# Performance work log

Hardware: AMD Instinct MI355X
Metric: run time of the kernel (lower is better)

## Reference

```python
import jax, jax.numpy as jnp
import numpy as np

N_QUBITS = 10
DIM = 2 ** N_QUBITS          # quantum state dimension
N_LAYERS = 8                 # QAOA circuit depth
B, D_IN, D_HID = 8192, 1024, 2048


def _build_hamiltonians(key):
    """Faithful to _create_cost_hamiltonian / _create_mixer_hamiltonian."""
    k1, k2 = jax.random.split(key)
    # cost: random diagonal * 0.1 plus 100 nearest-neighbour real couplings * 0.05
    diag = (jax.random.normal(k1, (DIM,)) * 0.1).astype(jnp.complex64)
    Hc = jnp.zeros((DIM, DIM), jnp.complex64).at[jnp.arange(DIM), jnp.arange(DIM)].set(diag)
    i = jnp.arange(100)
    j = (i + 1) % DIM
    c = (jax.random.normal(k2, (100,)) * 0.05).astype(jnp.complex64)
    Hc = Hc.at[i, j].set(c).at[j, i].set(jnp.conj(c))
    # mixer: sum of Pauli-X on every qubit -> H[i, i^(1<<q)] += 1
    idx = jnp.arange(DIM)
    Hm = jnp.zeros((DIM, DIM), jnp.complex64)
    for q in range(N_QUBITS):
        Hm = Hm.at[idx, idx ^ (1 << q)].add(1.0)
    return Hc, Hm


def setup_inputs() -> dict:
    key = jax.random.key(0)
    ks = jax.random.split(key, 8)
    Hc, Hm = _build_hamiltonians(ks[0])
    s = lambda k, *sh: jax.random.normal(k, sh, jnp.float32)
    return {
        "x": s(ks[1], B, D_IN),
        "W1": s(ks[2], D_IN, D_HID) * 0.02, "b1": jnp.zeros((D_HID,), jnp.float32),
        "W2": s(ks[3], D_HID, D_HID // 2) * 0.02, "b2": jnp.zeros((D_HID // 2,), jnp.float32),
        "Wq": s(ks[4], N_QUBITS, D_HID // 2) * 0.02, "bq": jnp.zeros((D_HID // 2,), jnp.float32),
        "Wo": s(ks[5], D_HID // 2, D_IN) * 0.02, "bo": jnp.zeros((D_IN,), jnp.float32),
        "circuit_params": s(ks[6], 2 * N_LAYERS),
        "Hc": Hc, "Hm": Hm,
    }


def _qaoa_params(circuit_params, Hc, Hm):
    """QuantumApproximateOptimizer.optimize_parameters: layered unitary evolution
    then a projective measurement mapped to +/-1 parameters."""
    state = jnp.full((DIM,), 1.0 / np.sqrt(DIM), jnp.complex64)
    for l in range(N_LAYERS):  # small fixed layer count -> Python loop OK
        gamma = circuit_params[2 * l].astype(jnp.complex64)
        beta = circuit_params[2 * l + 1].astype(jnp.complex64)
        state = jax.scipy.linalg.expm(-1j * gamma * Hc) @ state
        state = jax.scipy.linalg.expm(-1j * beta * Hm) @ state
    probs = jnp.abs(state) ** 2
    m = jax.random.categorical(jax.random.key(42), jnp.log(probs + 1e-30))
    # format(m, '0{n}b') is MSB-first
    bits = (m >> jnp.arange(N_QUBITS - 1, -1, -1)) & 1
    return bits.astype(jnp.float32) * 2.0 - 1.0  # +/-1 per qubit


def reference(x, W1, b1, W2, b2, Wq, bq, Wo, bo, circuit_params, Hc, Hm):
    # classical encoder: Linear -> ReLU -> Linear
    feat = jax.nn.relu(x @ W1 + b1) @ W2 + b2          # [B, D_HID//2]
    # quantum branch (batch independent)
    qp = _qaoa_params(circuit_params, Hc, Hm)          # [N_QUBITS]
    # surface-code error correction: correction_lookup only maps syndromes
    # '0000'/'1111' to qubit indices 23/24, which fail the `qubit_idx < param_dim`
    # guard for param_dim = N_QUBITS -> provably a no-op; qp unchanged.
    qf = qp @ Wq + bq                                  # [D_HID//2]
    return (feat + qf) @ Wo + bo                       # [B, D_IN]
```

## Files before the change

kernel.cpp:

```cpp
#include <hip/hip_runtime.h>
#include <hip/hip_bf16.h>
#include <stdint.h>

#define DIM 1024
#define NQ 10
#define NLAYERS 8
#define KTAYLOR 16
#define B_ROWS 8192
#define D_IN 1024
#define D_HID 2048
#define D_HALF 1024

typedef __bf16 bf16x8 __attribute__((ext_vector_type(8)));
typedef float f32x4 __attribute__((ext_vector_type(4)));

__device__ __forceinline__ float ldany(const void* p, size_t i, bool f32) {
  if (f32) return ((const float*)p)[i];
  return (float)((const __bf16*)p)[i];
}

__device__ __forceinline__ uint16_t f2bf_bits(float f) {
  __bf16 v = (__bf16)f;
  return *(uint16_t*)&v;
}

__global__ void detect_kernel(const uint32_t* __restrict__ w1raw,
                              const uint32_t* __restrict__ hc,
                              int* __restrict__ flags) {
  if (threadIdx.x == 0) {
    int cnt = 0;
    for (int i = 0; i < 256; ++i) {
      uint16_t h = (uint16_t)(w1raw[i] & 0xFFFFu);
      if (((h >> 7) & 0xFF) >= 0x80) cnt++;
    }
    flags[0] = (cnt > 32) ? 1 : 0;

    uint32_t w1 = hc[1] & 0x7FFFFFFFu;
    uint32_t w2 = hc[2] & 0x7FFFFFFFu;
    uint32_t w1025 = hc[1025] & 0x7FFFFFFFu;
    int code;
    if (w2 != 0u) code = 1;
    else if (w1 != 0u && (w1 >> 16) == 0u) code = 3;
    else if (w1025 != 0u) code = 2;
    else if (w1 != 0u) code = 4;
    else code = 0;
    flags[1] = code;
  }
}

__global__ __launch_bounds__(256) void convert_bf16(
    const void* __restrict__ src, size_t soff, __bf16* __restrict__ dst,
    int n, const int* __restrict__ flags) {
  int i = (blockIdx.x * 256 + threadIdx.x) * 8;
  if (i >= n) return;
  if (flags[0]) {
    const float* s = (const float*)src + soff + i;
#pragma unroll
    for (int j = 0; j < 8; ++j) dst[i + j] = (__bf16)s[j];
  } else {
    *(uint4*)(dst + i) = *(const uint4*)((const uint16_t*)src + soff + i);
  }
}

__device__ __forceinline__ uint32_t rotl32(uint32_t v, int d) {
  return (v << d) | (v >> (32 - d));
}

__device__ inline void threefry2x32(uint32_t k0, uint32_t k1, uint32_t& x0, uint32_t& x1) {
  uint32_t ks2 = k0 ^ k1 ^ 0x1BD11BDAu;
  x0 += k0; x1 += k1;
#define RND(r) { x0 += x1; x1 = rotl32(x1, r); x1 ^= x0; }
  RND(13) RND(15) RND(26) RND(6)
  x0 += k1; x1 += ks2 + 1u;
  RND(17) RND(29) RND(16) RND(24)
  x0 += ks2; x1 += k0 + 2u;
  RND(13) RND(15) RND(26) RND(6)
  x0 += k0; x1 += k1 + 3u;
  RND(17) RND(29) RND(16) RND(24)
  x0 += k1; x1 += ks2 + 4u;
  RND(13) RND(15) RND(26) RND(6)
  x0 += ks2; x1 += k0 + 5u;
#undef RND
}

__device__ __forceinline__ float gumbel_from_bits(uint32_t b) {
  float f = __uint_as_float((b >> 9) | 0x3f800000u) - 1.0f;
  float u = fmaxf(f, 1.17549435e-38f);
  return -__logf(-__logf(u));
}

struct cplx { double r, i; };
__device__ __forceinline__ cplx load_hc(const void* H, int code, size_t idx) {
  switch (code) {
    case 2: return {(double)((const float*)H)[idx], 0.0};
    case 3: {
      const uint16_t* h = (const uint16_t*)H;
      return {(double)__uint_as_float((uint32_t)h[2 * idx] << 16),
              (double)__uint_as_float((uint32_t)h[2 * idx + 1] << 16)};
    }
    case 4: {
      const double* d = (const double*)H;
      return {d[2 * idx], d[2 * idx + 1]};
    }
    default: {
      float2 v = ((const float2*)H)[idx];
      return {(double)v.x, (double)v.y};
    }
  }
}

__global__ __launch_bounds__(1024) void qaoa_kernel(
    const void* __restrict__ Hc_raw, const void* __restrict__ cp,
    const void* __restrict__ b1, const void* __restrict__ b2,
    const void* __restrict__ bq, const void* __restrict__ bo,
    const void* __restrict__ Wq, const int* __restrict__ flags,
    float* __restrict__ b1f, float* __restrict__ bias2, float* __restrict__ bof,
    int* __restrict__ diag) {
  __shared__ double2 Sb[2][DIM];
  __shared__ double gtab[NLAYERS], cbt[NLAYERS], sbt[NLAYERS];
  __shared__ float red_v[16];
  __shared__ int   red_i[16];
  __shared__ float red_p[16];
  __shared__ int bm_sh;

  const int t = threadIdx.x;
  const int lane = t & 63, wave = t >> 6;
  const bool f32 = (flags[0] != 0);
  const int code = flags[1];

  cplx dg = load_hc(Hc_raw, code, (size_t)t * DIM + t);

  cplx tdg0{0,0}, tdg1{0,0}, tcu0{0,0}, tcu1{0,0}, tcd0{0,0}, tcd1{0,0};
  if (wave == 0 && lane <= 50) {
    const size_t e0 = 2 * lane, e1 = 2 * lane + 1;
    tdg0 = load_hc(Hc_raw, code, e0 * DIM + e0);
    tdg1 = load_hc(Hc_raw, code, e1 * DIM + e1);
    if (e0 <= 100) tcu0 = load_hc(Hc_raw, code, e0 * DIM + e0 + 1);
    if (e1 <= 100) tcu1 = load_hc(Hc_raw, code, e1 * DIM + e1 + 1);
    if (e0 >= 1 && e0 <= 100) tcd0 = load_hc(Hc_raw, code, e0 * DIM + e0 - 1);
    if (e1 <= 100) tcd1 = load_hc(Hc_raw, code, e1 * DIM + e1 - 1);
  }

  if (t < NLAYERS) {
    gtab[t] = (double)ldany(cp, 2 * t, f32);
    double b = (double)ldany(cp, 2 * t + 1, f32);
    double s, c;
    sincos(b, &s, &c);
    cbt[t] = c; sbt[t] = s;
  }

  double ar = 0.03125, ai = 0.0;
  __syncthreads();

  for (int l = 0; l < NLAYERS; ++l) {
    const double gamma = gtab[l];
    const double cb = cbt[l], sb_ = sbt[l];

    Sb[0][t] = make_double2(ar, ai);
    __syncthreads();
    if (t >= 102) {
      float af_ = (float)(gamma * dg.r);
      double sn = (double)__sinf(af_), cs = (double)__cosf(af_);
      double sc_ = (dg.i == 0.0) ? 1.0 : exp(gamma * dg.i);
      double nr = sc_ * (ar * cs + ai * sn);
      double ni = sc_ * (ai * cs - ar * sn);
      ar = nr; ai = ni;
    } else if (wave == 0) {
      const double gd0r = gamma * tdg0.r, gd0i = gamma * tdg0.i;
      const double gd1r = gamma * tdg1.r, gd1i = gamma * tdg1.i;
      const double gu0r = gamma * tcu0.r, gu0i = gamma * tcu0.i;
      const double gu1r = gamma * tcu1.r, gu1i = gamma * tcu1.i;
      const double gc0r = gamma * tcd0.r, gc0i = gamma * tcd0.i;
      const double gc1r = gamma * tcd1.r, gc1i = gamma * tcd1.i;
      double p0r = 0, p0i = 0, p1r = 0, p1i = 0;
      if (lane <= 50) {
        double2 v0 = Sb[0][2 * lane], v1 = Sb[0][2 * lane + 1];
        p0r = v0.x; p0i = v0.y; p1r = v1.x; p1i = v1.y;
      }
      double y0r = p0r, y0i = p0i, y1r = p1r, y1i = p1i;
#pragma unroll
      for (int k = 1; k <= KTAYLOR; ++k) {
        double dnr = __shfl_up(p1r, 1), dni = __shfl_up(p1i, 1);
        double upr = __shfl_down(p0r, 1), upi = __shfl_down(p0i, 1);
        double h0r = gd0r * p0r - gd0i * p0i + gu0r * p1r - gu0i * p1i
                   + gc0r * dnr - gc0i * dni;
        double h0i = gd0r * p0i + gd0i * p0r + gu0r * p1i + gu0i * p1r
                   + gc0r * dni + gc0i * dnr;
        double h1r = gd1r * p1r - gd1i * p1i + gu1r * upr - gu1i * upi
                   + gc1r * p0r - gc1i * p0i;
        double h1i = gd1r * p1i + gd1i * p1r + gu1r * upi + gu1i * upr
                   + gc1r * p0i + gc1i * p0r;
        const double s = 1.0 / (double)k;
        p0r = s * h0i; p0i = -s * h0r;
        p1r = s * h1i; p1i = -s * h1r;
        y0r += p0r; y0i += p0i; y1r += p1r; y1i += p1i;
      }
      if (lane <= 50) {
        Sb[0][2 * lane]     = make_double2(y0r, y0i);
        Sb[0][2 * lane + 1] = make_double2(y1r, y1i);
      }
    }
    __syncthreads();
    if (t <= 101) { double2 v = Sb[0][t]; ar = v.x; ai = v.y; }

#pragma unroll
    for (int q = 0; q < 6; ++q) {
      double br_ = __shfl_xor(ar, 1 << q);
      double bi_ = __shfl_xor(ai, 1 << q);
      double nr = cb * ar + sb_ * bi_;
      double ni = cb * ai - sb_ * br_;
      ar = nr; ai = ni;
    }
    int s = 0;
#pragma unroll
    for (int q = 6; q < 10; ++q) {
      Sb[s][t] = make_double2(ar, ai);
      __syncthreads();
      double2 b = Sb[s][t ^ (1 << q)];
      double nr = cb * ar + sb_ * b.y;
      double ni = cb * ai - sb_ * b.x;
      ar = nr; ai = ni;
      s ^= 1;
    }
  }

  double prob = ar * ar + ai * ai;
  float pv = (float)prob;
  float score;
  {
    float logit = __logf((float)prob + 1e-30f);
    uint32_t x0 = 0u, x1 = (uint32_t)t;
    threefry2x32(0u, 42u, x0, x1);
    score = logit + gumbel_from_bits(x0 ^ x1);
  }
  int idx = t;
#pragma unroll
  for (int off = 32; off >= 1; off >>= 1) {
    float ov = __shfl_down(score, off);
    int oi = __shfl_down(idx, off);
    pv += __shfl_down(pv, off);
    if (ov > score) { score = ov; idx = oi; }
  }
  if (lane == 0) { red_v[wave] = score; red_i[wave] = idx; red_p[wave] = pv; }
  __syncthreads();
  if (t == 0) {
    float best = red_v[0]; int bm = red_i[0]; float total = red_p[0];
    for (int w = 1; w < 16; ++w) {
      total += red_p[w];
      if (red_v[w] > best) { best = red_v[w]; bm = red_i[w]; }
    }
    bm_sh = bm;
    diag[0] = (!(total > 0.99f && total < 1.01f)) ? 1 : 0;
    diag[1] = bm;
  }
  __syncthreads();
  const int m = bm_sh;

  float acc = ldany(b2, t, f32) + ldany(bq, t, f32);
#pragma unroll
  for (int k = 0; k < NQ; ++k) {
    float qp = ((m >> (9 - k)) & 1) ? 1.f : -1.f;
    acc += qp * ldany(Wq, k * D_HALF + t, f32);
  }
  bias2[t] = acc;
  bof[t] = ldany(bo, t, f32);
  b1f[t] = ldany(b1, t, f32);
  b1f[t + 1024] = ldany(b1, t + 1024, f32);
}

__global__ void sentinel_kernel(const int* __restrict__ flags,
                                const int* __restrict__ diag,
                                float* __restrict__ out) {
  if (threadIdx.x == 0 && (diag[0] || flags[1] == 0)) {
    out[0] = 1048576.0f + 4194304.0f * (float)diag[0]
           + 65536.0f * (float)flags[1] + 16.0f * (float)diag[1];
  }
}

__global__ __launch_bounds__(256) void transpose_any(
    const void* __restrict__ in, uint16_t* __restrict__ out, int R, int C,
    const int* __restrict__ flags) {
  __shared__ uint16_t tile[32][33];
  const bool f32 = (flags[0] != 0);
  int bc = blockIdx.x * 32, br = blockIdx.y * 32;
  int x = threadIdx.x, y = threadIdx.y;
#pragma unroll
  for (int i = 0; i < 4; ++i) {
    int r = y * 4 + i;
    size_t idx = (size_t)(br + r) * C + bc + x;
    tile[r][x] = f32 ? f2bf_bits(((const float*)in)[idx])
                     : ((const uint16_t*)in)[idx];
  }
  __syncthreads();
#pragma unroll
  for (int i = 0; i < 4; ++i) {
    int c = y * 4 + i;
    out[(size_t)(bc + c) * R + br + x] = tile[x][c];
  }
}

__device__ __forceinline__ void stage_tile(
    const __bf16* __restrict__ G, int row0, int K, int k0,
    __bf16* lds, int wave, int lane) {
#pragma unroll
  for (int r = 0; r < 2; ++r) {
    int e = r * 2048 + wave * 512 + lane * 8;
    int row = e >> 5, col = e & 31;
    const __bf16* gp = G + (size_t)(row0 + row) * K + k0 + col;
    __builtin_amdgcn_global_load_lds(
        (const __attribute__((address_space(1))) void*)gp,
        (__attribute__((address_space(3))) void*)(lds + r * 2048 + wave * 512),
        16, 0, 0);
  }
}

template <bool RELU, bool OUTF32>
__global__ __launch_bounds__(256) void gemm_bt(
    const __bf16* __restrict__ A, const __bf16* __restrict__ Bt,
    const float* __restrict__ bias, void* __restrict__ Cout,
    int N, int K) {
  __shared__ __bf16 Als[2][128 * 32];
  __shared__ __bf16 Bls[2][128 * 32];

  const int tid = threadIdx.x;
  const int wave = tid >> 6, lane = tid & 63;

  const int gx = gridDim.x;
  const int nwg = gx * gridDim.y;
  int flat = blockIdx.y * gx + blockIdx.x;
  const int chunk = nwg >> 3;
  flat = (flat & 7) * chunk + (flat >> 3);
  const int m0 = (flat / gx) * 128, n0 = (flat % gx) * 128;

  const int wm = (wave >> 1) * 64, wn = (wave & 1) * 64;
  const int lm = lane & 15, quad = lane >> 4;

  f32x4 acc[4][4] = {};

  const int nt = K >> 5;
  stage_tile(A,  m0, K, 0, Als[0], wave, lane);
  stage_tile(Bt, n0, K, 0, Bls[0], wave, lane);
  __syncthreads();

  for (int t = 0; t < nt; ++t) {
    const int cur = t & 1;
    if (t + 1 < nt) {
      stage_tile(A,  m0, K, (t + 1) << 5, Als[cur ^ 1], wave, lane);
      stage_tile(Bt, n0, K, (t + 1) << 5, Bls[cur ^ 1], wave, lane);
    }

    bf16x8 af[4], bfr[4];
#pragma unroll
    for (int i = 0; i < 4; ++i)
      af[i] = *(const bf16x8*)(Als[cur] + (wm + i * 16 + lm) * 32 + quad * 8);
#pragma unroll
    for (int i = 0; i < 4; ++i)
      bfr[i] = *(const bf16x8*)(Bls[cur] + (wn + i * 16 + lm) * 32 + quad * 8);

#pragma unroll
    for (int mi = 0; mi < 4; ++mi)
#pragma unroll
      for (int ni = 0; ni < 4; ++ni)
        acc[mi][ni] = __builtin_amdgcn_mfma_f32_16x16x32_bf16(
            af[mi], bfr[ni], acc[mi][ni], 0, 0, 0);

    __syncthreads();
  }

#pragma unroll
  for (int mi = 0; mi < 4; ++mi) {
#pragma unroll
    for (int ni = 0; ni < 4; ++ni) {
      int col = n0 + wn + ni * 16 + lm;
      float bv = bias[col];
#pragma unroll
      for (int r = 0; r < 4; ++r) {
        int row = m0 + wm + mi * 16 + quad * 4 + r;
        float v = acc[mi][ni][r] + bv;
        if (RELU) v = fmaxf(v, 0.f);
        size_t oi = (size_t)row * N + col;
        if (OUTF32) ((float*)Cout)[oi] = v;
        else        ((__bf16*)Cout)[oi] = (__bf16)v;
      }
    }
  }
}

extern "C" void kernel_launch(void* const* d_in, const int* in_sizes, int n_in,
                              void* d_out, int out_size, void* d_ws, size_t ws_size,
                              hipStream_t stream) {
  const void* x  = d_in[0];
  const void* W1 = d_in[1];
  const void* b1 = d_in[2];
  const void* W2 = d_in[3];
  const void* b2 = d_in[4];
  const void* Wq = d_in[5];
  const void* bq = d_in[6];
  const void* Wo = d_in[7];
  const void* bo = d_in[8];
  const void* cp = d_in[9];
  const void* Hc = d_in[10];
  float* out = (float*)d_out;

  char* ws = (char*)d_ws;
  float* b1f   = (float*)ws;
  float* bias2 = (float*)(ws + 8192);
  float* bof   = (float*)(ws + 12288);
  int*   flags = (int*)(ws + 16384);
  int*   diag  = (int*)(ws + 16384 + 64);
  __bf16* W1T = (__bf16*)(ws + 20480);
  __bf16* W2T = W1T + (size_t)2048 * 1024;
  __bf16* WoT = W2T + (size_t)2048 * 1024;
  const size_t head = 20480 + 10485760;
  int R = B_ROWS;
  while (R > 128 && head + (size_t)R * 8192 > ws_size) R >>= 1;
  __bf16* xc   = (__bf16*)(ws + head);
  __bf16* Hbuf = xc + (size_t)R * 1024;
  __bf16* Fbuf = Hbuf + (size_t)R * 2048;

  detect_kernel<<<1, 64, 0, stream>>>((const uint32_t*)W1, (const uint32_t*)Hc, flags);

  qaoa_kernel<<<1, 1024, 0, stream>>>(Hc, cp, b1, b2, bq, bo, Wq, flags,
                                      b1f, bias2, bof, diag);

  transpose_any<<<dim3(2048 / 32, 1024 / 32), dim3(32, 8), 0, stream>>>(
      W1, (uint16_t*)W1T, 1024, 2048, flags);
  transpose_any<<<dim3(1024 / 32, 2048 / 32), dim3(32, 8), 0, stream>>>(
      W2, (uint16_t*)W2T, 2048, 1024, flags);
  transpose_any<<<dim3(1024 / 32, 1024 / 32), dim3(32, 8), 0, stream>>>(
      Wo, (uint16_t*)WoT, 1024, 1024, flags);

  for (int off = 0; off < B_ROWS; off += R) {
    int nconv = R * 1024;
    convert_bf16<<<(nconv / 8 + 255) / 256, 256, 0, stream>>>(
        x, (size_t)off * D_IN, xc, nconv, flags);
    gemm_bt<true, false><<<dim3(D_HID / 128, R / 128), 256, 0, stream>>>(
        xc, W1T, b1f, Hbuf, D_HID, D_IN);
    gemm_bt<false, false><<<dim3(D_HALF / 128, R / 128), 256, 0, stream>>>(
        Hbuf, W2T, bias2, Fbuf, D_HALF, D_HID);
    gemm_bt<false, true><<<dim3(D_IN / 128, R / 128), 256, 0, stream>>>(
        Fbuf, WoT, bof, out + (size_t)off * D_IN, D_IN, D_HALF);
  }

  sentinel_kernel<<<1, 64, 0, stream>>>(flags, diag, out);
}
```

Before: 332.6 us.

## Fuse QAOA simulation into second GEMM launch as extra block with flag sync

```diff
diff --git a/kernel.cpp b/kernel.cpp
--- a/kernel.cpp
+++ b/kernel.cpp
@@ -22,44 +22,6 @@
 __device__ __forceinline__ uint16_t f2bf_bits(float f) {
   __bf16 v = (__bf16)f;
   return *(uint16_t*)&v;
-}
-
-__global__ void detect_kernel(const uint32_t* __restrict__ w1raw,
-                              const uint32_t* __restrict__ hc,
-                              int* __restrict__ flags) {
-  if (threadIdx.x == 0) {
-    int cnt = 0;
-    for (int i = 0; i < 256; ++i) {
-      uint16_t h = (uint16_t)(w1raw[i] & 0xFFFFu);
-      if (((h >> 7) & 0xFF) >= 0x80) cnt++;
-    }
-    flags[0] = (cnt > 32) ? 1 : 0;
-
-    uint32_t w1 = hc[1] & 0x7FFFFFFFu;
-    uint32_t w2 = hc[2] & 0x7FFFFFFFu;
-    uint32_t w1025 = hc[1025] & 0x7FFFFFFFu;
-    int code;
-    if (w2 != 0u) code = 1;
-    else if (w1 != 0u && (w1 >> 16) == 0u) code = 3;
-    else if (w1025 != 0u) code = 2;
-    else if (w1 != 0u) code = 4;
-    else code = 0;
-    flags[1] = code;
-  }
-}
-
-__global__ __launch_bounds__(256) void convert_bf16(
-    const void* __restrict__ src, size_t soff, __bf16* __restrict__ dst,
-    int n, const int* __restrict__ flags) {
-  int i = (blockIdx.x * 256 + threadIdx.x) * 8;
-  if (i >= n) return;
-  if (flags[0]) {
-    const float* s = (const float*)src + soff + i;
-#pragma unroll
-    for (int j = 0; j < 8; ++j) dst[i + j] = (__bf16)s[j];
-  } else {
-    *(uint4*)(dst + i) = *(const uint4*)((const uint16_t*)src + soff + i);
-  }
 }
 
 __device__ __forceinline__ uint32_t rotl32(uint32_t v, int d) {
@@ -109,163 +71,55 @@
   }
 }
 
-__global__ __launch_bounds__(1024) void qaoa_kernel(
-    const void* __restrict__ Hc_raw, const void* __restrict__ cp,
-    const void* __restrict__ b1, const void* __restrict__ b2,
-    const void* __restrict__ bq, const void* __restrict__ bo,
-    const void* __restrict__ Wq, const int* __restrict__ flags,
-    float* __restrict__ b1f, float* __restrict__ bias2, float* __restrict__ bof,
-    int* __restrict__ diag) {
-  __shared__ double2 Sb[2][DIM];
-  __shared__ double gtab[NLAYERS], cbt[NLAYERS], sbt[NLAYERS];
-  __shared__ float red_v[16];
-  __shared__ int   red_i[16];
-  __shared__ float red_p[16];
-  __shared__ int bm_sh;
-
+__global__ __launch_bounds__(1024) void detect_prep(
+    const uint32_t* __restrict__ w1raw, const uint32_t* __restrict__ hc,
+    const void* __restrict__ b1, const void* __restrict__ bo,
+    int* __restrict__ flags, float* __restrict__ b1f, float* __restrict__ bof,
+    int* __restrict__ qflag) {
+  __shared__ int cnt_sh;
+  __shared__ int f0_sh;
   const int t = threadIdx.x;
-  const int lane = t & 63, wave = t >> 6;
-  const bool f32 = (flags[0] != 0);
-  const int code = flags[1];
-
-  cplx dg = load_hc(Hc_raw, code, (size_t)t * DIM + t);
-
-  cplx tdg0{0,0}, tdg1{0,0}, tcu0{0,0}, tcu1{0,0}, tcd0{0,0}, tcd1{0,0};
-  if (wave == 0 && lane <= 50) {
-    const size_t e0 = 2 * lane, e1 = 2 * lane + 1;
-    tdg0 = load_hc(Hc_raw, code, e0 * DIM + e0);
-    tdg1 = load_hc(Hc_raw, code, e1 * DIM + e1);
-    if (e0 <= 100) tcu0 = load_hc(Hc_raw, code, e0 * DIM + e0 + 1);
-    if (e1 <= 100) tcu1 = load_hc(Hc_raw, code, e1 * DIM + e1 + 1);
-    if (e0 >= 1 && e0 <= 100) tcd0 = load_hc(Hc_raw, code, e0 * DIM + e0 - 1);
-    if (e1 <= 100) tcd1 = load_hc(Hc_raw, code, e1 * DIM + e1 - 1);
-  }
-
-  if (t < NLAYERS) {
-    gtab[t] = (double)ldany(cp, 2 * t, f32);
-    double b = (double)ldany(cp, 2 * t + 1, f32);
-    double s, c;
-    sincos(b, &s, &c);
-    cbt[t] = c; sbt[t] = s;
-  }
-
-  double ar = 0.03125, ai = 0.0;
-  __syncthreads();
-
-  for (int l = 0; l < NLAYERS; ++l) {
-    const double gamma = gtab[l];
-    const double cb = cbt[l], sb_ = sbt[l];
-
-    Sb[0][t] = make_double2(ar, ai);
-    __syncthreads();
-    if (t >= 102) {
-      float af_ = (float)(gamma * dg.r);
-      double sn = (double)__sinf(af_), cs = (double)__cosf(af_);
-      double sc_ = (dg.i == 0.0) ? 1.0 : exp(gamma * dg.i);
-      double nr = sc_ * (ar * cs + ai * sn);
-      double ni = sc_ * (ai * cs - ar * sn);
-      ar = nr; ai = ni;
-    } else if (wave == 0) {
-      const double gd0r = gamma * tdg0.r, gd0i = gamma * tdg0.i;
-      const double gd1r = gamma * tdg1.r, gd1i = gamma * tdg1.i;
-      const double gu0r = gamma * tcu0.r, gu0i = gamma * tcu0.i;
-      const double gu1r = gamma * tcu1.r, gu1i = gamma * tcu1.i;
-      const double gc0r = gamma * tcd0.r, gc0i = gamma * tcd0.i;
-      const double gc1r = gamma * tcd1.r, gc1i = gamma * tcd1.i;
-      double p0r = 0, p0i = 0, p1r = 0, p1i = 0;
-      if (lane <= 50) {
-        double2 v0 = Sb[0][2 * lane], v1 = Sb[0][2 * lane + 1];
-        p0r = v0.x; p0i = v0.y; p1r = v1.x; p1i = v1.y;
-      }
-      double y0r = p0r, y0i = p0i, y1r = p1r, y1i = p1i;
-#pragma unroll
-      for (int k = 1; k <= KTAYLOR; ++k) {
-        double dnr = __shfl_up(p1r, 1), dni = __shfl_up(p1i, 1);
-        double upr = __shfl_down(p0r, 1), upi = __shfl_down(p0i, 1);
-        double h0r = gd0r * p0r - gd0i * p0i + gu0r * p1r - gu0i * p1i
-                   + gc0r * dnr - gc0i * dni;
-        double h0i = gd0r * p0i + gd0i * p0r + gu0r * p1i + gu0i * p1r
-                   + gc0r * dni + gc0i * dnr;
-        double h1r = gd1r * p1r - gd1i * p1i + gu1r * upr - gu1i * upi
-                   + gc1r * p0r - gc1i * p0i;
-        double h1i = gd1r * p1i + gd1i * p1r + gu1r * upi + gu1i * upr
-                   + gc1r * p0i + gc1i * p0r;
-        const double s = 1.0 / (double)k;
-        p0r = s * h0i; p0i = -s * h0r;
-        p1r = s * h1i; p1i = -s * h1r;
-        y0r += p0r; y0i += p0i; y1r += p1r; y1i += p1i;
-      }
-      if (lane <= 50) {
-        Sb[0][2 * lane]     = make_double2(y0r, y0i);
-        Sb[0][2 * lane + 1] = make_double2(y1r, y1i);
-      }
-    }
-    __syncthreads();
-    if (t <= 101) { double2 v = Sb[0][t]; ar = v.x; ai = v.y; }
-
-#pragma unroll
-    for (int q = 0; q < 6; ++q) {
-      double br_ = __shfl_xor(ar, 1 << q);
-      double bi_ = __shfl_xor(ai, 1 << q);
-      double nr = cb * ar + sb_ * bi_;
-      double ni = cb * ai - sb_ * br_;
-      ar = nr; ai = ni;
-    }
-    int s = 0;
-#pragma unroll
-    for (int q = 6; q < 10; ++q) {
-      Sb[s][t] = make_double2(ar, ai);
-      __syncthreads();
-      double2 b = Sb[s][t ^ (1 << q)];
-      double nr = cb * ar + sb_ * b.y;
-      double ni = cb * ai - sb_ * b.x;
-      ar = nr; ai = ni;
-      s ^= 1;
-    }
-  }
-
-  double prob = ar * ar + ai * ai;
-  float pv = (float)prob;
-  float score;
-  {
-    float logit = __logf((float)prob + 1e-30f);
-    uint32_t x0 = 0u, x1 = (uint32_t)t;
-    threefry2x32(0u, 42u, x0, x1);
-    score = logit + gumbel_from_bits(x0 ^ x1);
-  }
-  int idx = t;
-#pragma unroll
-  for (int off = 32; off >= 1; off >>= 1) {
-    float ov = __shfl_down(score, off);
-    int oi = __shfl_down(idx, off);
-    pv += __shfl_down(pv, off);
-    if (ov > score) { score = ov; idx = oi; }
-  }
-  if (lane == 0) { red_v[wave] = score; red_i[wave] = idx; red_p[wave] = pv; }
+  if (t == 0) cnt_sh = 0;
+  __syncthreads();
+  if (t < 256) {
+    uint16_t h = (uint16_t)(w1raw[t] & 0xFFFFu);
+    if (((h >> 7) & 0xFF) >= 0x80) atomicAdd(&cnt_sh, 1);
+  }
   __syncthreads();
   if (t == 0) {
-    float best = red_v[0]; int bm = red_i[0]; float total = red_p[0];
-    for (int w = 1; w < 16; ++w) {
-      total += red_p[w];
-      if (red_v[w] > best) { best = red_v[w]; bm = red_i[w]; }
-    }
-    bm_sh = bm;
-    diag[0] = (!(total > 0.99f && total < 1.01f)) ? 1 : 0;
-    diag[1] = bm;
-  }
-  __syncthreads();
-  const int m = bm_sh;
-
-  float acc = ldany(b2, t, f32) + ldany(bq, t, f32);
-#pragma unroll
-  for (int k = 0; k < NQ; ++k) {
-    float qp = ((m >> (9 - k)) & 1) ? 1.f : -1.f;
-    acc += qp * ldany(Wq, k * D_HALF + t, f32);
-  }
-  bias2[t] = acc;
-  bof[t] = ldany(bo, t, f32);
+    f0_sh = (cnt_sh > 32) ? 1 : 0;
+    flags[0] = f0_sh;
+    uint32_t w1 = hc[1] & 0x7FFFFFFFu;
+    uint32_t w2 = hc[2] & 0x7FFFFFFFu;
+    uint32_t w1025 = hc[1025] & 0x7FFFFFFFu;
+    int code;
+    if (w2 != 0u) code = 1;
+    else if (w1 != 0u && (w1 >> 16) == 0u) code = 3;
+    else if (w1025 != 0u) code = 2;
+    else if (w1 != 0u) code = 4;
+    else code = 0;
+    flags[1] = code;
+    qflag[0] = 0;
+  }
+  __syncthreads();
+  const bool f32 = (f0_sh != 0);
   b1f[t] = ldany(b1, t, f32);
   b1f[t + 1024] = ldany(b1, t + 1024, f32);
+  bof[t] = ldany(bo, t, f32);
+}
+
+__global__ __launch_bounds__(256) void convert_bf16(
+    const void* __restrict__ src, size_t soff, __bf16* __restrict__ dst,
+    int n, const int* __restrict__ flags) {
+  int i = (blockIdx.x * 256 + threadIdx.x) * 8;
+  if (i >= n) return;
+  if (flags[0]) {
+    const float* s = (const float*)src + soff + i;
+#pragma unroll
+    for (int j = 0; j < 8; ++j) dst[i + j] = (__bf16)s[j];
+  } else {
+    *(uint4*)(dst + i) = *(const uint4*)((const uint16_t*)src + soff + i);
+  }
 }
 
 __global__ void sentinel_kernel(const int* __restrict__ flags,
@@ -297,6 +151,191 @@
     int c = y * 4 + i;
     out[(size_t)(bc + c) * R + br + x] = tile[x][c];
   }
+}
+
+__device__ void qaoa_body(char* smem,
+    const void* __restrict__ Hc_raw, const void* __restrict__ cp,
+    const void* __restrict__ b2, const void* __restrict__ bq,
+    const void* __restrict__ Wq, const int* __restrict__ flags,
+    float* __restrict__ bias2, int* __restrict__ diag,
+    int* __restrict__ qflag) {
+  double2* X   = (double2*)smem;
+  double* gtab = (double*)(smem + 16384);
+  double* cbt  = gtab + 8;
+  double* sbt  = cbt + 8;
+  float* redv  = (float*)(sbt + 8);
+  float* redp  = redv + 4;
+  int*   redi  = (int*)(redp + 4);
+  int*   bmsh  = redi + 4;
+
+  const int t = threadIdx.x;
+  const int lane = t & 63, w = t >> 6;
+  const bool f32 = (flags[0] != 0);
+  const int code = flags[1];
+
+  double dgr[4], dgi[4];
+#pragma unroll
+  for (int j = 0; j < 4; ++j) {
+    size_t e = (size_t)(w * 256 + j * 64 + lane);
+    cplx d = load_hc(Hc_raw, code, e * DIM + e);
+    dgr[j] = d.r; dgi[j] = d.i;
+  }
+  double u0r = 0, u0i = 0, c0r = 0, c0i = 0;
+  double u1r = 0, u1i = 0, c1r = 0, c1i = 0;
+  if (w == 0) {
+    const int e0 = lane, e1 = 64 + lane;
+    { cplx u = load_hc(Hc_raw, code, (size_t)e0 * DIM + e0 + 1); u0r = u.r; u0i = u.i; }
+    if (e0 >= 1)  { cplx c = load_hc(Hc_raw, code, (size_t)e0 * DIM + e0 - 1); c0r = c.r; c0i = c.i; }
+    if (e1 <= 100){ cplx u = load_hc(Hc_raw, code, (size_t)e1 * DIM + e1 + 1); u1r = u.r; u1i = u.i; }
+    if (e1 <= 101){ cplx c = load_hc(Hc_raw, code, (size_t)e1 * DIM + e1 - 1); c1r = c.r; c1i = c.i; }
+  }
+  if (t < NLAYERS) {
+    gtab[t] = (double)ldany(cp, 2 * t, f32);
+    double b = (double)ldany(cp, 2 * t + 1, f32), s, c;
+    sincos(b, &s, &c);
+    cbt[t] = c; sbt[t] = s;
+  }
+  double ar[4], ai[4];
+#pragma unroll
+  for (int j = 0; j < 4; ++j) { ar[j] = 0.03125; ai[j] = 0.0; }
+  __syncthreads();
+
+  for (int l = 0; l < NLAYERS; ++l) {
+    const double gamma = gtab[l];
+    const double cb = cbt[l], sb = sbt[l];
+
+    if (w == 0) {
+      double p0r = ar[0], p0i = ai[0], p1r = ar[1], p1i = ai[1];
+      double y0r = p0r, y0i = p0i, y1r = p1r, y1i = p1i;
+#pragma unroll 4
+      for (int k = 1; k <= KTAYLOR; ++k) {
+        double a0r = __shfl_down(p0r, 1), a0i = __shfl_down(p0i, 1);
+        double a1r = __shfl_down(p1r, 1), a1i = __shfl_down(p1i, 1);
+        double m0r = __shfl_up(p0r, 1),   m0i = __shfl_up(p0i, 1);
+        double m1r = __shfl_up(p1r, 1),   m1i = __shfl_up(p1i, 1);
+        double b0r = __shfl(p1r, 0),  b0i = __shfl(p1i, 0);
+        double b1r = __shfl(p0r, 63), b1i = __shfl(p0i, 63);
+        if (lane == 63) { a0r = b0r; a0i = b0i; }
+        if (lane == 0)  { m1r = b1r; m1i = b1i; }
+        double h0r = dgr[0]*p0r - dgi[0]*p0i + u0r*a0r - u0i*a0i + c0r*m0r - c0i*m0i;
+        double h0i = dgr[0]*p0i + dgi[0]*p0r + u0r*a0i + u0i*a0r + c0r*m0i + c0i*m0r;
+        double h1r = dgr[1]*p1r - dgi[1]*p1i + u1r*a1r - u1i*a1i + c1r*m1r - c1i*m1i;
+        double h1i = dgr[1]*p1i + dgi[1]*p1r + u1r*a1i + u1i*a1r + c1r*m1i + c1i*m1r;
+        double s = gamma / (double)k;
+        p0r = s * h0i; p0i = -s * h0r;
+        p1r = s * h1i; p1i = -s * h1r;
+        y0r += p0r; y0i += p0i; y1r += p1r; y1i += p1i;
+      }
+      ar[0] = y0r; ai[0] = y0i; ar[1] = y1r; ai[1] = y1i;
+#pragma unroll
+      for (int j = 2; j < 4; ++j) {
+        float angf = (float)(gamma * dgr[j]);
+        double sn = (double)__sinf(angf), cs = (double)__cosf(angf);
+        double sc_ = (dgi[j] == 0.0) ? 1.0 : exp(gamma * dgi[j]);
+        double nr = sc_ * (ar[j] * cs + ai[j] * sn);
+        double ni = sc_ * (ai[j] * cs - ar[j] * sn);
+        ar[j] = nr; ai[j] = ni;
+      }
+    } else {
+#pragma unroll
+      for (int j = 0; j < 4; ++j) {
+        float angf = (float)(gamma * dgr[j]);
+        double sn = (double)__sinf(angf), cs = (double)__cosf(angf);
+        double sc_ = (dgi[j] == 0.0) ? 1.0 : exp(gamma * dgi[j]);
+        double nr = sc_ * (ar[j] * cs + ai[j] * sn);
+        double ni = sc_ * (ai[j] * cs - ar[j] * sn);
+        ar[j] = nr; ai[j] = ni;
+      }
+    }
+
+#pragma unroll
+    for (int q = 0; q < 6; ++q) {
+      const int msk = 1 << q;
+#pragma unroll
+      for (int j = 0; j < 4; ++j) {
+        double pr = __shfl_xor(ar[j], msk), pi = __shfl_xor(ai[j], msk);
+        double nr = cb * ar[j] + sb * pi;
+        double ni = cb * ai[j] - sb * pr;
+        ar[j] = nr; ai[j] = ni;
+      }
+    }
+    {
+      const double cb2 = cb * cb, cbsb = cb * sb, sb2 = sb * sb;
+      double nr[4], ni[4];
+#pragma unroll
+      for (int j = 0; j < 4; ++j) {
+        nr[j] = cb2 * ar[j] + cbsb * (ai[j ^ 1] + ai[j ^ 2]) - sb2 * ar[j ^ 3];
+        ni[j] = cb2 * ai[j] - cbsb * (ar[j ^ 1] + ar[j ^ 2]) - sb2 * ai[j ^ 3];
+      }
+#pragma unroll
+      for (int j = 0; j < 4; ++j) { ar[j] = nr[j]; ai[j] = ni[j]; }
+    }
+    {
+#pragma unroll
+      for (int j = 0; j < 4; ++j)
+        X[w * 256 + j * 64 + lane] = make_double2(ar[j], ai[j]);
+      __syncthreads();
+      const double cb2 = cb * cb, cbsb = cb * sb, sb2 = sb * sb;
+#pragma unroll
+      for (int j = 0; j < 4; ++j) {
+        int e = w * 256 + j * 64 + lane;
+        double2 vb = X[e ^ 256], vc = X[e ^ 512], vd = X[e ^ 768];
+        double nr = cb2 * ar[j] + cbsb * (vb.y + vc.y) - sb2 * vd.x;
+        double ni = cb2 * ai[j] - cbsb * (vb.x + vc.x) - sb2 * vd.y;
+        ar[j] = nr; ai[j] = ni;
+      }
+      __syncthreads();
+    }
+  }
+
+  float best = -1e30f; int bidx = 0; float pv = 0.f;
+#pragma unroll
+  for (int j = 0; j < 4; ++j) {
+    int e = w * 256 + j * 64 + lane;
+    double prob = ar[j] * ar[j] + ai[j] * ai[j];
+    pv += (float)prob;
+    float logit = __logf((float)prob + 1e-30f);
+    uint32_t x0 = 0u, x1 = (uint32_t)e;
+    threefry2x32(0u, 42u, x0, x1);
+    float sc = logit + gumbel_from_bits(x0 ^ x1);
+    if (sc > best) { best = sc; bidx = e; }
+  }
+#pragma unroll
+  for (int off = 32; off >= 1; off >>= 1) {
+    float ov = __shfl_down(best, off);
+    int oi = __shfl_down(bidx, off);
+    pv += __shfl_down(pv, off);
+    if (ov > best) { best = ov; bidx = oi; }
+  }
+  if (lane == 0) { redv[w] = best; redi[w] = bidx; redp[w] = pv; }
+  __syncthreads();
+  if (t == 0) {
+    float bb = redv[0]; int bm = redi[0]; float tot = redp[0];
+    for (int k = 1; k < 4; ++k) {
+      tot += redp[k];
+      if (redv[k] > bb) { bb = redv[k]; bm = redi[k]; }
+    }
+    bmsh[0] = bm;
+    diag[0] = (!(tot > 0.99f && tot < 1.01f)) ? 1 : 0;
+    diag[1] = bm;
+  }
+  __syncthreads();
+  const int m = bmsh[0];
+
+#pragma unroll
+  for (int k4 = 0; k4 < 4; ++k4) {
+    int c = t + 256 * k4;
+    float acc = ldany(b2, c, f32) + ldany(bq, c, f32);
+#pragma unroll
+    for (int k = 0; k < NQ; ++k) {
+      float qp = ((m >> (9 - k)) & 1) ? 1.f : -1.f;
+      acc += qp * ldany(Wq, (size_t)k * D_HALF + c, f32);
+    }
+    bias2[c] = acc;
+  }
+  __syncthreads();
+  if (t == 0)
+    __hip_atomic_store(qflag, 1, __ATOMIC_RELEASE, __HIP_MEMORY_SCOPE_AGENT);
 }
 
 __device__ __forceinline__ void stage_tile(
@@ -348,7 +387,6 @@
       stage_tile(A,  m0, K, (t + 1) << 5, Als[cur ^ 1], wave, lane);
       stage_tile(Bt, n0, K, (t + 1) << 5, Bls[cur ^ 1], wave, lane);
     }
-
     bf16x8 af[4], bfr[4];
 #pragma unroll
     for (int i = 0; i < 4; ++i)
@@ -356,14 +394,12 @@
 #pragma unroll
     for (int i = 0; i < 4; ++i)
       bfr[i] = *(const bf16x8*)(Bls[cur] + (wn + i * 16 + lm) * 32 + quad * 8);
-
 #pragma unroll
     for (int mi = 0; mi < 4; ++mi)
 #pragma unroll
       for (int ni = 0; ni < 4; ++ni)
         acc[mi][ni] = __builtin_amdgcn_mfma_f32_16x16x32_bf16(
             af[mi], bfr[ni], acc[mi][ni], 0, 0, 0);
-
     __syncthreads();
   }
 
@@ -381,6 +417,88 @@
         size_t oi = (size_t)row * N + col;
         if (OUTF32) ((float*)Cout)[oi] = v;
         else        ((__bf16*)Cout)[oi] = (__bf16)v;
+      }
+    }
+  }
+}
+
+__global__ __launch_bounds__(256, 4) void gemm2_fused(
+    const __bf16* __restrict__ A, const __bf16* __restrict__ Bt,
+    void* __restrict__ Cout, int N, int K, int ntiles,
+    const void* __restrict__ Hc_raw, const void* __restrict__ cp,
+    const void* __restrict__ b2, const void* __restrict__ bq,
+    const void* __restrict__ Wq, const int* __restrict__ flags,
+    float* __restrict__ bias2, int* __restrict__ diag,
+    int* __restrict__ qflag) {
+  __shared__ __align__(16) char smem[33024];
+
+  if (blockIdx.x == 0) {
+    qaoa_body(smem, Hc_raw, cp, b2, bq, Wq, flags, bias2, diag, qflag);
+    return;
+  }
+
+  __bf16* Als = (__bf16*)smem;
+  __bf16* Bls = (__bf16*)(smem + 16384);
+
+  const int tid = threadIdx.x;
+  const int wave = tid >> 6, lane = tid & 63;
+
+  int flat = blockIdx.x - 1;
+  const int gx = N >> 7;
+  const int chunk = ntiles >> 3;
+  flat = (flat & 7) * chunk + (flat >> 3);
+  const int m0 = (flat / gx) * 128, n0 = (flat % gx) * 128;
+
+  const int wm = (wave >> 1) * 64, wn = (wave & 1) * 64;
+  const int lm = lane & 15, quad = lane >> 4;
+
+  f32x4 acc[4][4] = {};
+
+  const int nt = K >> 5;
+  stage_tile(A,  m0, K, 0, Als, wave, lane);
+  stage_tile(Bt, n0, K, 0, Bls, wave, lane);
+  __syncthreads();
+
+  for (int t = 0; t < nt; ++t) {
+    const int cur = t & 1;
+    if (t + 1 < nt) {
+      stage_tile(A,  m0, K, (t + 1) << 5, Als + (cur ^ 1) * 4096, wave, lane);
+      stage_tile(Bt, n0, K, (t + 1) << 5, Bls + (cur ^ 1) * 4096, wave, lane);
+    }
+    bf16x8 af[4], bfr[4];
+#pragma unroll
+    for (int i = 0; i < 4; ++i)
+      af[i] = *(const bf16x8*)(Als + cur * 4096 + (wm + i * 16 + lm) * 32 + quad * 8);
+#pragma unroll
+    for (int i = 0; i < 4; ++i)
+      bfr[i] = *(const bf16x8*)(Bls + cur * 4096 + (wn + i * 16 + lm) * 32 + quad * 8);
+#pragma unroll
+    for (int mi = 0; mi < 4; ++mi)
+#pragma unroll
+      for (int ni = 0; ni < 4; ++ni)
+        acc[mi][ni] = __builtin_amdgcn_mfma_f32_16x16x32_bf16(
+            af[mi], bfr[ni], acc[mi][ni], 0, 0, 0);
+    __syncthreads();
+  }
+
+  if (tid == 0) {
+    while (__hip_atomic_load(qflag, __ATOMIC_ACQUIRE, __HIP_MEMORY_SCOPE_AGENT) == 0)
+      __builtin_amdgcn_s_sleep(2);
+  }
+  __syncthreads();
+
+#pragma unroll
+  for (int mi = 0; mi < 4; ++mi) {
+#pragma unroll
+    for (int ni = 0; ni < 4; ++ni) {
+      int col = n0 + wn + ni * 16 + lm;
+      float bv = bias2[col];
+#pragma unroll
+      for (int r = 0; r < 4; ++r) {
+        int row = m0 + wm + mi * 16 + quad * 4 + r;
+        float v = acc[mi][ni][r] + bv;
+        size_t oi = (size_t)row * N + col;
+        ((__bf16*)Cout)[oi] = (__bf16)v;
       }
     }
   }
@@ -408,6 +526,7 @@
   float* bof   = (float*)(ws + 12288);
   int*   flags = (int*)(ws + 16384);
   int*   diag  = (int*)(ws + 16384 + 64);
+  int*   qflag = (int*)(ws + 16384 + 128);
   __bf16* W1T = (__bf16*)(ws + 20480);
   __bf16* W2T = W1T + (size_t)2048 * 1024;
   __bf16* WoT = W2T + (size_t)2048 * 1024;
@@ -418,10 +537,8 @@
   __bf16* Hbuf = xc + (size_t)R * 1024;
   __bf16* Fbuf = Hbuf + (size_t)R * 2048;
 
-  detect_kernel<<<1, 64, 0, stream>>>((const uint32_t*)W1, (const uint32_t*)Hc, flags);
-
-  qaoa_kernel<<<1, 1024, 0, stream>>>(Hc, cp, b1, b2, bq, bo, Wq, flags,
-                                      b1f, bias2, bof, diag);
+  detect_prep<<<1, 1024, 0, stream>>>((const uint32_t*)W1, (const uint32_t*)Hc,
+                                      b1, bo, flags, b1f, bof, qflag);
 
   transpose_any<<<dim3(2048 / 32, 1024 / 32), dim3(32, 8), 0, stream>>>(
       W1, (uint16_t*)W1T, 1024, 2048, flags);
@@ -436,8 +553,15 @@
         x, (size_t)off * D_IN, xc, nconv, flags);
     gemm_bt<true, false><<<dim3(D_HID / 128, R / 128), 256, 0, stream>>>(
         xc, W1T, b1f, Hbuf, D_HID, D_IN);
-    gemm_bt<false, false><<<dim3(D_HALF / 128, R / 128), 256, 0, stream>>>(
-        Hbuf, W2T, bias2, Fbuf, D_HALF, D_HID);
+    if (off == 0) {
+      int ntiles = (D_HALF / 128) * (R / 128);
+      gemm2_fused<<<ntiles + 1, 256, 0, stream>>>(
+          Hbuf, W2T, Fbuf, D_HALF, D_HID, ntiles,
+          Hc, cp, b2, bq, Wq, flags, bias2, diag, qflag);
+    } else {
+      gemm_bt<false, false><<<dim3(D_HALF / 128, R / 128), 256, 0, stream>>>(
+          Hbuf, W2T, bias2, Fbuf, D_HALF, D_HID);
+    }
     gemm_bt<false, true><<<dim3(D_IN / 128, R / 128), 256, 0, stream>>>(
         Fbuf, WoT, bof, out + (size_t)off * D_IN, D_IN, D_HALF);
   }
```

Measured after the change: 307.4 us. 1.08x faster.
